# Optimization experiments

Measured on AMD Instinct MI355X. Metric: run time of the kernel, lower is better.

The kernel has to match this reference:

```python
import jax, jax.numpy as jnp
import numpy as np

B, N, D = 16, 2048, 128  # batch, nodes, embedding_dim

def setup_inputs() -> dict:
    key = jax.random.key(0)
    ks = jax.random.split(key, 12)
    def dense(kw, kb, din, dout):
        # keras Dense default glorot_uniform weight, zeros bias (use small random bias for generality)
        lim = np.sqrt(6.0 / (din + dout))
        W = jax.random.uniform(kw, (din, dout), minval=-lim, maxval=lim, dtype=jnp.float32)
        b = jax.random.normal(kb, (dout,), dtype=jnp.float32) * 0.01
        return W, b
    Wq, bq = dense(ks[0], ks[1], D, D)
    Wk, bk = dense(ks[2], ks[3], D, D)
    Wv, bv = dense(ks[4], ks[5], D, D)
    Wo, bo = dense(ks[6], ks[7], D, D)
    query_ = jax.random.normal(ks[8], (B, N, D), dtype=jnp.float32)
    key_ = jax.random.normal(ks[9], (B, N, D), dtype=jnp.float32)
    mask = jax.random.randint(ks[10], (B, N + 1, N + 1), 0, 2).astype(bool)
    return {"query_": query_, "key_": key_, "mask": mask,
            "Wq": Wq, "bq": bq, "Wk": Wk, "bk": bk,
            "Wv": Wv, "bv": bv, "Wo": Wo, "bo": bo}

def reference(query_, key_, mask, Wq, bq, Wk, bk, Wv, bv, Wo, bo):
    q = query_ @ Wq + bq                       # [B,N,D]
    k = key_ @ Wk + bk                         # [B,N,D]
    comp = jnp.einsum('bqd,bkd->bqk', q, k)    # [B,N,N]
    comp = comp / jnp.sqrt(jnp.asarray(k.shape[-1], jnp.float32))
    m = mask[:, 1:, 1:]                        # [B,N,N]
    comp = jnp.where(m, -jnp.inf, comp)
    attn = jax.nn.softmax(comp, axis=-1)
    attn = jnp.where(jnp.isnan(attn), 0.0, attn)  # fully-masked rows -> 0
    # NOTE: faithful to source: value projection applied to the PROJECTED key
    v = k @ Wv + bv                            # [B,N,D]
    out = jnp.einsum('bqk,bkd->bqd', attn, v)
    return out @ Wo + bo
```

## Files before the change

kernel.cpp:

```cpp
#include <hip/hip_runtime.h>

#define SB 16
#define SN 2048
#define SD 128
#define NM 2049
#define SZ (SB*SN*SD)

typedef __bf16 bf16x8 __attribute__((ext_vector_type(8)));
typedef float f32x4 __attribute__((ext_vector_type(4)));

__device__ __forceinline__ unsigned short f2b(float f){
  union { float f; unsigned int u; } v; v.f = f;
  unsigned int r = v.u + 0x7fffu + ((v.u >> 16) & 1u);
  return (unsigned short)(r >> 16);
}

__device__ __forceinline__ void async16(const void* g, void* l){
  __builtin_amdgcn_global_load_lds(
      (__attribute__((address_space(1))) void*)(g),
      (__attribute__((address_space(3))) void*)(l), 16, 0, 0);
}

__global__ __launch_bounds__(256) void prep_w_kernel(
    const float* __restrict__ Wq, const float* __restrict__ Wk,
    const float* __restrict__ Wv, const float* __restrict__ Wo,
    unsigned short* __restrict__ out)
{
  int widx = blockIdx.x >> 4;
  int kg   = blockIdx.x & 15;
  const float* W = (widx==0)?Wq:(widx==1)?Wk:(widx==2)?Wv:Wo;
  unsigned short* O = out + widx*16384;
  int t = threadIdx.x;
  int k = kg*8 + (t>>5);
  int n = (t&31)*4;
  float4 v = *reinterpret_cast<const float4*>(W + k*SD + n);
  O[(n+0)*SD + k] = f2b(v.x);
  O[(n+1)*SD + k] = f2b(v.y);
  O[(n+2)*SD + k] = f2b(v.z);
  O[(n+3)*SD + k] = f2b(v.w);
}

__global__ __launch_bounds__(256,4) void qkv_kernel(
    const float* __restrict__ query, const float* __restrict__ key,
    const unsigned short* __restrict__ wts,
    const float* __restrict__ bq, const float* __restrict__ bk,
    const float* __restrict__ bv,
    unsigned short* __restrict__ qb, unsigned short* __restrict__ kb,
    unsigned short* __restrict__ vt)
{
  __shared__ unsigned short kstrip[2][16*136];
  __shared__ unsigned short vT[SD*40];

  int tid=threadIdx.x;
  int w=tid>>6, ln=tid&63, g=ln>>4, lm=ln&15;
  int b = blockIdx.x >> 6, nt = blockIdx.x & 63;
  int n0 = nt*32;
  size_t rowbase = (size_t)b*SN + n0;
  const float sc = 0.08838834764831845f;

  const unsigned short* WqT = wts;
  const unsigned short* WkT = wts + 16384;
  const unsigned short* WvT = wts + 32768;

  if (w < 2){
    const float* xr = query + (rowbase + w*16 + lm)*SD;
    bf16x8 af[4];
    for (int ks=0;ks<4;ks++){
      float4 x0 = *reinterpret_cast<const float4*>(xr + ks*32 + g*8);
      float4 x1 = *reinterpret_cast<const float4*>(xr + ks*32 + g*8 + 4);
      union { bf16x8 v; unsigned short s[8]; } u;
      u.s[0]=f2b(x0.x); u.s[1]=f2b(x0.y); u.s[2]=f2b(x0.z); u.s[3]=f2b(x0.w);
      u.s[4]=f2b(x1.x); u.s[5]=f2b(x1.y); u.s[6]=f2b(x1.z); u.s[7]=f2b(x1.w);
      af[ks]=u.v;
    }
    for (int d=0; d<8; d++){
      f32x4 acc = {0.f,0.f,0.f,0.f};
      for (int ks=0;ks<4;ks++){
        bf16x8 wf = *reinterpret_cast<const bf16x8*>(WqT + (d*16+lm)*SD + ks*32 + g*8);
        acc = __builtin_amdgcn_mfma_f32_16x16x32_bf16(af[ks], wf, acc, 0,0,0);
      }
      float bb = bq[d*16+lm];
      for (int r=0;r<4;r++)
        qb[(rowbase + w*16 + 4*g + r)*SD + d*16 + lm] = f2b((acc[r]+bb)*sc);
    }
  } else {
    int wv = w-2;
    const float* xr = key + (rowbase + wv*16 + lm)*SD;
    bf16x8 af[4];
    for (int ks=0;ks<4;ks++){
      float4 x0 = *reinterpret_cast<const float4*>(xr + ks*32 + g*8);
      float4 x1 = *reinterpret_cast<const float4*>(xr + ks*32 + g*8 + 4);
      union { bf16x8 v; unsigned short s[8]; } u;
      u.s[0]=f2b(x0.x); u.s[1]=f2b(x0.y); u.s[2]=f2b(x0.z); u.s[3]=f2b(x0.w);
      u.s[4]=f2b(x1.x); u.s[5]=f2b(x1.y); u.s[6]=f2b(x1.z); u.s[7]=f2b(x1.w);
      af[ks]=u.v;
    }
    unsigned short* ks_ = kstrip[wv];
    for (int d=0; d<8; d++){
      f32x4 acc = {0.f,0.f,0.f,0.f};
      for (int ks=0;ks<4;ks++){
        bf16x8 wf = *reinterpret_cast<const bf16x8*>(WkT + (d*16+lm)*SD + ks*32 + g*8);
        acc = __builtin_amdgcn_mfma_f32_16x16x32_bf16(af[ks], wf, acc, 0,0,0);
      }
      float bb = bk[d*16+lm];
      for (int r=0;r<4;r++){
        unsigned short kv = f2b(acc[r]+bb);
        kb[(rowbase + wv*16 + 4*g + r)*SD + d*16 + lm] = kv;
        ks_[(4*g+r)*136 + d*16 + lm] = kv;
      }
    }
    bf16x8 ka[4];
    for (int ks=0;ks<4;ks++)
      ka[ks] = *reinterpret_cast<const bf16x8*>(&ks_[lm*136 + ks*32 + g*8]);
    for (int d=0; d<8; d++){
      f32x4 acc = {0.f,0.f,0.f,0.f};
      for (int ks=0;ks<4;ks++){
        bf16x8 wf = *reinterpret_cast<const bf16x8*>(WvT + (d*16+lm)*SD + ks*32 + g*8);
        acc = __builtin_amdgcn_mfma_f32_16x16x32_bf16(ka[ks], wf, acc, 0,0,0);
      }
      float bb = bv[d*16+lm];
      ushort4 pk;
      pk.x=f2b(acc[0]+bb); pk.y=f2b(acc[1]+bb);
      pk.z=f2b(acc[2]+bb); pk.w=f2b(acc[3]+bb);
      *reinterpret_cast<ushort4*>(&vT[(d*16+lm)*40 + wv*16 + 4*g]) = pk;
    }
  }
  __syncthreads();
  int d = tid>>1, half = tid&1;
  const uint4* src = reinterpret_cast<const uint4*>(&vT[d*40 + half*16]);
  uint4* dst = reinterpret_cast<uint4*>(vt + (size_t)b*SD*SN + (size_t)d*SN + n0 + half*16);
  dst[0]=src[0]; dst[1]=src[1];
}

__global__ __launch_bounds__(256,4) void flash_kernel(
    const unsigned short* __restrict__ qb, const unsigned short* __restrict__ kb,
    const unsigned short* __restrict__ vt, const int* __restrict__ mask,
    const unsigned short* __restrict__ WoT, const float* __restrict__ bo,
    float* __restrict__ out)
{
  __shared__ unsigned short bufK[2][64*128];
  __shared__ unsigned short bufV[2][128*64];
  __shared__ unsigned short ldsP[4*16*72];

  int tid=threadIdx.x;
  int w=tid>>6, ln=tid&63, g=ln>>4, lm=ln&15;
  int b = blockIdx.x >> 5, qt = blockIdx.x & 31;
  int q0 = qt*64;

  const unsigned short* Qb = qb + (size_t)b*SN*SD;
  const unsigned short* Kb = kb + (size_t)b*SN*SD;
  const unsigned short* Vb = vt + (size_t)b*SD*SN;
  const int* Mb = mask + (size_t)b*NM*NM;

  auto issueK = [&](int k0, int bi){
    const char* gbase = (const char*)Kb + (size_t)k0*256;
    for (int c=0;c<4;c++){
      int p = c*256 + tid;
      int row = p>>4, lc = (p&15) ^ (row&15);
      async16(gbase + (size_t)row*256 + lc*16, (char*)bufK[bi] + p*16);
    }
  };
  auto issueV = [&](int k0, int bi){
    const char* gbase = (const char*)Vb + (size_t)k0*2;
    for (int c=0;c<4;c++){
      int p = c*256 + tid;
      int row = p>>3, lc = (p&7) ^ (row&7);
      async16(gbase + (size_t)row*4096 + lc*16, (char*)bufV[bi] + p*16);
    }
  };

  issueK(0,0); issueV(0,0);

  bf16x8 qf[4];
  {
    const unsigned short* qr = Qb + (size_t)(q0 + w*16 + lm)*SD;
    for (int ks=0;ks<4;ks++)
      qf[ks] = *reinterpret_cast<const bf16x8*>(qr + ks*32 + g*8);
  }

  int qr1 = 1 + q0 + w*16 + 4*g;
  const int* mbase = Mb + (size_t)qr1*NM + 1 + lm;
  int mreg[16];
  for (int ct=0;ct<4;ct++)
    for (int r=0;r<4;r++)
      mreg[ct*4+r] = mbase[(size_t)r*NM + ct*16];

  float mrow[4], lrow[4], al[4];
  f32x4 acc[8];
  for (int r=0;r<4;r++){ mrow[r]=-INFINITY; lrow[r]=0.f; }
  for (int d=0;d<8;d++){ f32x4 z={0.f,0.f,0.f,0.f}; acc[d]=z; }
  unsigned short* pw = &ldsP[w*16*72];

  for (int kt=0; kt<32; kt++){
    __syncthreads();
    int cur = kt&1;
    if (kt<31){ issueK((kt+1)*64, cur^1); issueV((kt+1)*64, cur^1); }

    f32x4 s[4];
    for (int ct=0;ct<4;ct++){
      f32x4 z = {0.f,0.f,0.f,0.f};
      for (int ks=0;ks<4;ks++){
        bf16x8 kf = *reinterpret_cast<const bf16x8*>(
            &bufK[cur][(ct*16+lm)*128 + (((ks*4+g)^lm))*8]);
        z = __builtin_amdgcn_mfma_f32_16x16x32_bf16(qf[ks], kf, z, 0,0,0);
      }
      s[ct]=z;
    }

    for (int ct=0;ct<4;ct++)
      for (int r=0;r<4;r++)
        s[ct][r] = mreg[ct*4+r] ? -INFINITY : s[ct][r];
    if (kt<31){
      const int* mp = mbase + (kt+1)*64;
      for (int ct=0;ct<4;ct++)
        for (int r=0;r<4;r++)
          mreg[ct*4+r] = mp[(size_t)r*NM + ct*16];
    }

    for (int r=0;r<4;r++){
      float v = fmaxf(fmaxf(s[0][r],s[1][r]), fmaxf(s[2][r],s[3][r]));
      v = fmaxf(v, __shfl_xor(v,1,16));
      v = fmaxf(v, __shfl_xor(v,2,16));
      v = fmaxf(v, __shfl_xor(v,4,16));
      v = fmaxf(v, __shfl_xor(v,8,16));
      float mn = fmaxf(mrow[r], v);
      bool dead = (mn == -INFINITY);
      float a = dead ? 1.f : __expf(mrow[r]-mn);
      float rsum = 0.f;
      for (int ct=0;ct<4;ct++){
        float p = dead ? 0.f : __expf(s[ct][r]-mn);
        s[ct][r]=p; rsum += p;
      }
      rsum += __shfl_xor(rsum,1,16);
      rsum += __shfl_xor(rsum,2,16);
      rsum += __shfl_xor(rsum,4,16);
      rsum += __shfl_xor(rsum,8,16);
      lrow[r] = lrow[r]*a + rsum;
      mrow[r] = mn;
      al[r] = a;
    }
    for (int d=0;d<8;d++)
      for (int r=0;r<4;r++)
        acc[d][r] *= al[r];

    for (int ct=0;ct<4;ct++){
      int col = ct*16+lm;
      for (int r=0;r<4;r++)
        pw[(4*g+r)*72 + col] = f2b(s[ct][r]);
    }
    bf16x8 pa0 = *reinterpret_cast<const bf16x8*>(&pw[lm*72 + g*8]);
    bf16x8 pa1 = *reinterpret_cast<const bf16x8*>(&pw[lm*72 + 32 + g*8]);

    for (int d=0;d<8;d++){
      bf16x8 v0 = *reinterpret_cast<const bf16x8*>(
          &bufV[cur][(d*16+lm)*64 + ((g^(lm&7)))*8]);
      acc[d] = __builtin_amdgcn_mfma_f32_16x16x32_bf16(pa0, v0, acc[d], 0,0,0);
      bf16x8 v1 = *reinterpret_cast<const bf16x8*>(
          &bufV[cur][(d*16+lm)*64 + (((4+g)^(lm&7)))*8]);
      acc[d] = __builtin_amdgcn_mfma_f32_16x16x32_bf16(pa1, v1, acc[d], 0,0,0);
    }
  }

  __syncthreads();
  float inv[4];
  for (int r=0;r<4;r++) inv[r] = (lrow[r] > 0.f) ? (1.f/lrow[r]) : 0.f;
  unsigned short* strip = &bufK[0][0] + w*2176;
  for (int d=0;d<8;d++)
    for (int r=0;r<4;r++)
      strip[(4*g+r)*136 + d*16 + lm] = f2b(acc[d][r]*inv[r]);
  bf16x8 oa[4];
  for (int ks=0;ks<4;ks++)
    oa[ks] = *reinterpret_cast<const bf16x8*>(&strip[lm*136 + ks*32 + g*8]);
  float* Ob = out + ((size_t)b*SN + q0 + w*16)*SD;
  for (int dc=0; dc<8; dc++){
    f32x4 o = {0.f,0.f,0.f,0.f};
    for (int ks=0;ks<4;ks++){
      bf16x8 wf = *reinterpret_cast<const bf16x8*>(WoT + (dc*16+lm)*SD + ks*32 + g*8);
      o = __builtin_amdgcn_mfma_f32_16x16x32_bf16(oa[ks], wf, o, 0,0,0);
    }
    float bb = bo[dc*16+lm];
    for (int r=0;r<4;r++)
      Ob[(size_t)(4*g+r)*SD + dc*16 + lm] = o[r]+bb;
  }
}

extern "C" void kernel_launch(void* const* d_in, const int* in_sizes, int n_in,
                              void* d_out, int out_size, void* d_ws, size_t ws_size,
                              hipStream_t stream)
{
  const float* query = (const float*)d_in[0];
  const float* key   = (const float*)d_in[1];
  const int*   mask  = (const int*)d_in[2];
  const float* Wq = (const float*)d_in[3];
  const float* bq = (const float*)d_in[4];
  const float* Wk = (const float*)d_in[5];
  const float* bk = (const float*)d_in[6];
  const float* Wv = (const float*)d_in[7];
  const float* bv = (const float*)d_in[8];
  const float* Wo = (const float*)d_in[9];
  const float* bo = (const float*)d_in[10];
  float* out = (float*)d_out;

  unsigned short* qb = (unsigned short*)d_ws;
  unsigned short* kb = qb + SZ;
  unsigned short* vt = kb + SZ;
  unsigned short* wts = vt + SZ;

  prep_w_kernel<<<64,256,0,stream>>>(Wq,Wk,Wv,Wo,wts);
  qkv_kernel  <<<1024,256,0,stream>>>(query, key, wts, bq, bk, bv, qb, kb, vt);
  flash_kernel<<<512,256,0,stream>>>(qb, kb, vt, mask, wts+49152, bo, out);
}
```

Before: 490.8 us.

## Fold Wk·Wv into a combined weight, remap flash blocks per XCD, add priorities

Adds a prep kernel that precomputes Wk@Wv and bk@Wv+bv so V is computed directly from the key input, removing the dependent K→V chain and its LDS staging in the QKV kernel. The QKV kernel is restructured so each wave handles one 16-row tile, writing V transposed straight to global memory. The flash kernel also remaps block IDs so each XCD handles two whole batches (for K/V L2 locality), marks mask loads and output stores nontemporal, and raises wave priority around the MFMA loops. The combined weight is rounded to bf16 once, which changes rounding relative to the two-step projection. The strided scalar V stores may be less coalesced than before.

New measurement: 500.7 us. 2.0% more time.

```diff
diff --git a/kernel.cpp b/kernel.cpp
--- a/kernel.cpp
+++ b/kernel.cpp
@@ -40,30 +40,50 @@
   O[(n+3)*SD + k] = f2b(v.w);
 }
 
+__global__ __launch_bounds__(256) void prep_wkv_kernel(
+    const float* __restrict__ Wk, const float* __restrict__ Wv,
+    const float* __restrict__ bk, const float* __restrict__ bv,
+    unsigned short* __restrict__ WkvT, float* __restrict__ bkv)
+{
+  int t = threadIdx.x;
+  int k = blockIdx.x*8 + (t>>5);
+  int n0 = (t&31)*4;
+  float ax=0.f, ay=0.f, az=0.f, aw=0.f;
+  for (int m=0;m<SD;m++){
+    float wk = Wk[k*SD+m];
+    float4 wv = *reinterpret_cast<const float4*>(Wv + m*SD + n0);
+    ax += wk*wv.x; ay += wk*wv.y; az += wk*wv.z; aw += wk*wv.w;
+  }
+  WkvT[(n0+0)*SD + k] = f2b(ax);
+  WkvT[(n0+1)*SD + k] = f2b(ay);
+  WkvT[(n0+2)*SD + k] = f2b(az);
+  WkvT[(n0+3)*SD + k] = f2b(aw);
+  if (blockIdx.x==0 && t < SD){
+    float a = 0.f;
+    for (int m=0;m<SD;m++) a += bk[m]*Wv[m*SD + t];
+    bkv[t] = a + bv[t];
+  }
+}
+
 __global__ __launch_bounds__(256,4) void qkv_kernel(
     const float* __restrict__ query, const float* __restrict__ key,
     const unsigned short* __restrict__ wts,
     const float* __restrict__ bq, const float* __restrict__ bk,
-    const float* __restrict__ bv,
+    const float* __restrict__ bkv,
     unsigned short* __restrict__ qb, unsigned short* __restrict__ kb,
     unsigned short* __restrict__ vt)
 {
-  __shared__ unsigned short kstrip[2][16*136];
-  __shared__ unsigned short vT[SD*40];
-
   int tid=threadIdx.x;
   int w=tid>>6, ln=tid&63, g=ln>>4, lm=ln&15;
-  int b = blockIdx.x >> 6, nt = blockIdx.x & 63;
-  int n0 = nt*32;
-  size_t rowbase = (size_t)b*SN + n0;
-  const float sc = 0.08838834764831845f;
-
-  const unsigned short* WqT = wts;
-  const unsigned short* WkT = wts + 16384;
-  const unsigned short* WvT = wts + 32768;
-
-  if (w < 2){
-    const float* xr = query + (rowbase + w*16 + lm)*SD;
+  int wr = (w + ((blockIdx.x & 1) << 1)) & 3;
+  int id = blockIdx.x*2 + (wr & 1);
+  int b = id >> 7, nt = id & 127;
+  size_t rowbase = (size_t)b*SN + nt*16;
+
+  if (wr < 2){
+    const unsigned short* WkT  = wts + 16384;
+    const unsigned short* WkvT = wts + 32768;
+    const float* xr = key + (rowbase + lm)*SD;
     bf16x8 af[4];
     for (int ks=0;ks<4;ks++){
       float4 x0 = *reinterpret_cast<const float4*>(xr + ks*32 + g*8);
@@ -76,16 +96,30 @@
     for (int d=0; d<8; d++){
       f32x4 acc = {0.f,0.f,0.f,0.f};
       for (int ks=0;ks<4;ks++){
-        bf16x8 wf = *reinterpret_cast<const bf16x8*>(WqT + (d*16+lm)*SD + ks*32 + g*8);
+        bf16x8 wf = *reinterpret_cast<const bf16x8*>(WkT + (d*16+lm)*SD + ks*32 + g*8);
         acc = __builtin_amdgcn_mfma_f32_16x16x32_bf16(af[ks], wf, acc, 0,0,0);
       }
-      float bb = bq[d*16+lm];
-      for (int r=0;r<4;r++)
-        qb[(rowbase + w*16 + 4*g + r)*SD + d*16 + lm] = f2b((acc[r]+bb)*sc);
+      float bb = bk[d*16+lm];
+      for (int r=0;r<4;r++)
+        kb[(rowbase + 4*g + r)*SD + d*16 + lm] = f2b(acc[r]+bb);
+    }
+    unsigned short* vcol = vt + (size_t)b*SD*SN + nt*16 + lm;
+    for (int d=0; d<8; d++){
+      f32x4 acc = {0.f,0.f,0.f,0.f};
+      for (int ks=0;ks<4;ks++){
+        bf16x8 wf = *reinterpret_cast<const bf16x8*>(WkvT + (d*16+lm)*SD + ks*32 + g*8);
+        acc = __builtin_amdgcn_mfma_f32_16x16x32_bf16(wf, af[ks], acc, 0,0,0);
+      }
+      float4 bb = *reinterpret_cast<const float4*>(bkv + d*16 + 4*g);
+      vcol[(size_t)(d*16 + 4*g + 0)*SN] = f2b(acc[0]+bb.x);
+      vcol[(size_t)(d*16 + 4*g + 1)*SN] = f2b(acc[1]+bb.y);
+      vcol[(size_t)(d*16 + 4*g + 2)*SN] = f2b(acc[2]+bb.z);
+      vcol[(size_t)(d*16 + 4*g + 3)*SN] = f2b(acc[3]+bb.w);
     }
   } else {
-    int wv = w-2;
-    const float* xr = key + (rowbase + wv*16 + lm)*SD;
+    const unsigned short* WqT = wts;
+    const float sc = 0.08838834764831845f;
+    const float* xr = query + (rowbase + lm)*SD;
     bf16x8 af[4];
     for (int ks=0;ks<4;ks++){
       float4 x0 = *reinterpret_cast<const float4*>(xr + ks*32 + g*8);
@@ -95,41 +129,17 @@
       u.s[4]=f2b(x1.x); u.s[5]=f2b(x1.y); u.s[6]=f2b(x1.z); u.s[7]=f2b(x1.w);
       af[ks]=u.v;
     }
-    unsigned short* ks_ = kstrip[wv];
     for (int d=0; d<8; d++){
       f32x4 acc = {0.f,0.f,0.f,0.f};
       for (int ks=0;ks<4;ks++){
-        bf16x8 wf = *reinterpret_cast<const bf16x8*>(WkT + (d*16+lm)*SD + ks*32 + g*8);
+        bf16x8 wf = *reinterpret_cast<const bf16x8*>(WqT + (d*16+lm)*SD + ks*32 + g*8);
         acc = __builtin_amdgcn_mfma_f32_16x16x32_bf16(af[ks], wf, acc, 0,0,0);
       }
-      float bb = bk[d*16+lm];
-      for (int r=0;r<4;r++){
-        unsigned short kv = f2b(acc[r]+bb);
-        kb[(rowbase + wv*16 + 4*g + r)*SD + d*16 + lm] = kv;
-        ks_[(4*g+r)*136 + d*16 + lm] = kv;
-      }
-    }
-    bf16x8 ka[4];
-    for (int ks=0;ks<4;ks++)
-      ka[ks] = *reinterpret_cast<const bf16x8*>(&ks_[lm*136 + ks*32 + g*8]);
-    for (int d=0; d<8; d++){
-      f32x4 acc = {0.f,0.f,0.f,0.f};
-      for (int ks=0;ks<4;ks++){
-        bf16x8 wf = *reinterpret_cast<const bf16x8*>(WvT + (d*16+lm)*SD + ks*32 + g*8);
-        acc = __builtin_amdgcn_mfma_f32_16x16x32_bf16(ka[ks], wf, acc, 0,0,0);
-      }
-      float bb = bv[d*16+lm];
-      ushort4 pk;
-      pk.x=f2b(acc[0]+bb); pk.y=f2b(acc[1]+bb);
-      pk.z=f2b(acc[2]+bb); pk.w=f2b(acc[3]+bb);
-      *reinterpret_cast<ushort4*>(&vT[(d*16+lm)*40 + wv*16 + 4*g]) = pk;
-    }
-  }
-  __syncthreads();
-  int d = tid>>1, half = tid&1;
-  const uint4* src = reinterpret_cast<const uint4*>(&vT[d*40 + half*16]);
-  uint4* dst = reinterpret_cast<uint4*>(vt + (size_t)b*SD*SN + (size_t)d*SN + n0 + half*16);
-  dst[0]=src[0]; dst[1]=src[1];
+      float bb = bq[d*16+lm];
+      for (int r=0;r<4;r++)
+        qb[(rowbase + 4*g + r)*SD + d*16 + lm] = f2b((acc[r]+bb)*sc);
+    }
+  }
 }
 
 __global__ __launch_bounds__(256,4) void flash_kernel(
@@ -144,7 +154,10 @@
 
   int tid=threadIdx.x;
   int w=tid>>6, ln=tid&63, g=ln>>4, lm=ln&15;
-  int b = blockIdx.x >> 5, qt = blockIdx.x & 31;
+  int xcd   = blockIdx.x & 7;
+  int inner = blockIdx.x >> 3;
+  int b  = xcd*2 + (inner>>5);
+  int qt = inner & 31;
   int q0 = qt*64;
 
   const unsigned short* Qb = qb + (size_t)b*SN*SD;
@@ -183,7 +196,7 @@
   int mreg[16];
   for (int ct=0;ct<4;ct++)
     for (int r=0;r<4;r++)
-      mreg[ct*4+r] = mbase[(size_t)r*NM + ct*16];
+      mreg[ct*4+r] = __builtin_nontemporal_load(mbase + (size_t)r*NM + ct*16);
 
   float mrow[4], lrow[4], al[4];
   f32x4 acc[8];
@@ -197,6 +210,7 @@
     if (kt<31){ issueK((kt+1)*64, cur^1); issueV((kt+1)*64, cur^1); }
 
     f32x4 s[4];
+    __builtin_amdgcn_s_setprio(1);
     for (int ct=0;ct<4;ct++){
       f32x4 z = {0.f,0.f,0.f,0.f};
       for (int ks=0;ks<4;ks++){
@@ -206,6 +220,7 @@
       }
       s[ct]=z;
     }
+    __builtin_amdgcn_s_setprio(0);
 
     for (int ct=0;ct<4;ct++)
       for (int r=0;r<4;r++)
@@ -214,7 +229,7 @@
       const int* mp = mbase + (kt+1)*64;
       for (int ct=0;ct<4;ct++)
         for (int r=0;r<4;r++)
-          mreg[ct*4+r] = mp[(size_t)r*NM + ct*16];
+          mreg[ct*4+r] = __builtin_nontemporal_load(mp + (size_t)r*NM + ct*16);
     }
 
     for (int r=0;r<4;r++){
@@ -251,6 +266,7 @@
     bf16x8 pa0 = *reinterpret_cast<const bf16x8*>(&pw[lm*72 + g*8]);
     bf16x8 pa1 = *reinterpret_cast<const bf16x8*>(&pw[lm*72 + 32 + g*8]);
 
+    __builtin_amdgcn_s_setprio(1);
     for (int d=0;d<8;d++){
       bf16x8 v0 = *reinterpret_cast<const bf16x8*>(
           &bufV[cur][(d*16+lm)*64 + ((g^(lm&7)))*8]);
@@ -259,6 +275,7 @@
           &bufV[cur][(d*16+lm)*64 + (((4+g)^(lm&7)))*8]);
       acc[d] = __builtin_amdgcn_mfma_f32_16x16x32_bf16(pa1, v1, acc[d], 0,0,0);
     }
+    __builtin_amdgcn_s_setprio(0);
   }
 
   __syncthreads();
@@ -280,7 +297,7 @@
     }
     float bb = bo[dc*16+lm];
     for (int r=0;r<4;r++)
-      Ob[(size_t)(4*g+r)*SD + dc*16 + lm] = o[r]+bb;
+      __builtin_nontemporal_store(o[r]+bb, &Ob[(size_t)(4*g+r)*SD + dc*16 + lm]);
   }
 }
 
@@ -305,8 +322,10 @@
   unsigned short* kb = qb + SZ;
   unsigned short* vt = kb + SZ;
   unsigned short* wts = vt + SZ;
-
-  prep_w_kernel<<<64,256,0,stream>>>(Wq,Wk,Wv,Wo,wts);
-  qkv_kernel  <<<1024,256,0,stream>>>(query, key, wts, bq, bk, bv, qb, kb, vt);
-  flash_kernel<<<512,256,0,stream>>>(qb, kb, vt, mask, wts+49152, bo, out);
-}
+  float* bkv = (float*)(wts + 65536);
+
+  prep_w_kernel  <<<64,256,0,stream>>>(Wq,Wk,Wv,Wo,wts);
+  prep_wkv_kernel<<<16,256,0,stream>>>(Wk,Wv,bk,bv, wts+32768, bkv);
+  qkv_kernel     <<<1024,256,0,stream>>>(query, key, wts, bq, bk, bkv, qb, kb, vt);
+  flash_kernel   <<<512,256,0,stream>>>(qb, kb, vt, mask, wts+49152, bo, out);
+}
```
